# Kernel tuning notes

Hardware: AMD Instinct MI355X
Metric: run time of the kernel (lower is better)

Reference implementation:

```python
import jax, jax.numpy as jnp
import numpy as np

D_MODEL = 1024
NUM_HEADS = 16
HEAD_DIM = D_MODEL // NUM_HEADS
BATCH, SEQ = 2, 2048


def setup_inputs() -> dict:
    key = jax.random.key(0)
    ks = jax.random.split(key, 11)
    s = 1.0 / np.sqrt(D_MODEL)
    inp = {
        "query": jax.random.normal(ks[0], (BATCH, SEQ, D_MODEL), jnp.float32),
        "key": jax.random.normal(ks[1], (BATCH, SEQ, D_MODEL), jnp.float32),
        "value": jax.random.normal(ks[2], (BATCH, SEQ, D_MODEL), jnp.float32),
        "q_w": jax.random.uniform(ks[3], (D_MODEL, D_MODEL), jnp.float32, -s, s),
        "q_b": jax.random.uniform(ks[4], (D_MODEL,), jnp.float32, -s, s),
        "k_w": jax.random.uniform(ks[5], (D_MODEL, D_MODEL), jnp.float32, -s, s),
        "k_b": jax.random.uniform(ks[6], (D_MODEL,), jnp.float32, -s, s),
        "v_w": jax.random.uniform(ks[7], (D_MODEL, D_MODEL), jnp.float32, -s, s),
        "v_b": jax.random.uniform(ks[8], (D_MODEL,), jnp.float32, -s, s),
        "o_w": jax.random.uniform(ks[9], (D_MODEL, D_MODEL), jnp.float32, -s, s),
        "o_b": jax.random.uniform(ks[10], (D_MODEL,), jnp.float32, -s, s),
    }
    return inp


def reference(query, key, value, q_w, q_b, k_w, k_b, v_w, v_b, o_w, o_b):
    B = query.shape[0]
    # linear projections (torch Linear: x @ W^T + b)
    q = query @ q_w.T + q_b
    k = key @ k_w.T + k_b
    v = value @ v_w.T + v_b
    # split heads: [B, S, D] -> [B, H, S, Hd]
    def split(x):
        return x.reshape(B, -1, NUM_HEADS, HEAD_DIM).transpose(0, 2, 1, 3)
    q, k, v = split(q), split(k), split(v)
    scores = jnp.einsum("bhqd,bhkd->bhqk", q, k) / np.sqrt(HEAD_DIM).astype(np.float32)
    attn = jax.nn.softmax(scores, axis=-1)
    out = jnp.einsum("bhqk,bhkd->bhqd", attn, v)  # [B,H,S,Hd]
    merged = out.transpose(0, 2, 1, 3).reshape(B, -1, D_MODEL)
    return merged @ o_w.T + o_b
```

## Files before the change

### kernel.cpp

```cpp
#include <hip/hip_runtime.h>
#include <hip/hip_bf16.h>

typedef unsigned short u16;
typedef unsigned int u32;
typedef __attribute__((ext_vector_type(8))) short short8;
typedef __attribute__((ext_vector_type(4))) short s16x4;
typedef __attribute__((ext_vector_type(4))) float f32x4;
typedef __attribute__((ext_vector_type(4))) u32 u32v4;

__device__ __forceinline__ u16 f2bf(float f) {
    u32 u = __float_as_uint(f);
    return (u16)((u + 0x7FFFu + ((u >> 16) & 1u)) >> 16);
}
__device__ __forceinline__ u32 pack2bf(float a, float b) {
    __hip_bfloat162 h = __float22bfloat162_rn(float2{a, b});
    return *reinterpret_cast<u32*>(&h);
}
__device__ __forceinline__ float exp2hw(float x) {
    float r;
    asm("v_exp_f32 %0, %1" : "=v"(r) : "v"(x));
    return r;
}

__device__ __forceinline__ void gload16(const void* g, void* s) {
    __builtin_amdgcn_global_load_lds(
        (const __attribute__((address_space(1))) void*)g,
        (__attribute__((address_space(3))) void*)s, 16, 0, 0);
}

__global__ __launch_bounds__(256) void cast_w_kernel(
    const float* __restrict__ s0, const float* __restrict__ s1,
    const float* __restrict__ s2, const float* __restrict__ s3,
    u16* __restrict__ d0, u16* __restrict__ d1, u16* __restrict__ d2,
    u16* __restrict__ d3, int n)
{
    const int y = blockIdx.y;
    const float* s = y == 0 ? s0 : (y == 1 ? s1 : (y == 2 ? s2 : s3));
    u16* d = y == 0 ? d0 : (y == 1 ? d1 : (y == 2 ? d2 : d3));
    int i = (blockIdx.x * 256 + threadIdx.x) * 4;
    if (i < n) {
        float4 v = *(const float4*)(s + i);
        uint2 t;
        t.x = pack2bf(v.x, v.y);
        t.y = pack2bf(v.z, v.w);
        *(uint2*)(d + i) = t;
    }
}

__global__ __launch_bounds__(256) void qkv_gemm(
    const float* __restrict__ Xq, const float* __restrict__ Xk, const float* __restrict__ Xv,
    const u16* __restrict__ Wq, const u16* __restrict__ Wk, const u16* __restrict__ Wv,
    const float* __restrict__ qb, const float* __restrict__ kb, const float* __restrict__ vb,
    u16* __restrict__ Qo, u16* __restrict__ Ko, u16* __restrict__ Vo)
{
    constexpr int N = 1024, K = 1024;
    __shared__ __align__(16) u16 Asm[2][4096];
    __shared__ __align__(16) u16 Bsm[2][4096];
    const int z = blockIdx.z;
    const float* Afp = z == 0 ? Xq : (z == 1 ? Xk : Xv);
    const u16* W = z == 0 ? Wq : (z == 1 ? Wk : Wv);
    const float* bias = z == 0 ? qb : (z == 1 ? kb : vb);

    const int tid = threadIdx.x;
    const int wid = tid >> 6;
    const int lane = tid & 63;
    const int r15 = lane & 15, g = lane >> 4;
    const int fb = blockIdx.y * 8 + blockIdx.x;
    const int lsw = (fb & 7) * 32 + (fb >> 3);
    const int m0 = (lsw >> 3) * 128, n0 = (lsw & 7) * 128;
    const int wr = wid >> 1, wc = wid & 1;

    f32x4 acc[4][4];
#pragma unroll
    for (int i = 0; i < 4; ++i)
#pragma unroll
        for (int j = 0; j < 4; ++j) acc[i][j] = (f32x4){0.f, 0.f, 0.f, 0.f};

    const float* Abase = Afp + (size_t)(m0 + (tid >> 3)) * 1024 + (tid & 7) * 4;
    const int wboff = (tid >> 3) * 32 + (tid & 7) * 4;
    const int idx0 = tid, idx1 = tid + 256;
    const size_t boff0 = (size_t)(n0 + (idx0 >> 2)) * K + (idx0 & 3) * 8;
    const size_t boff1 = (size_t)(n0 + (idx1 >> 2)) * K + (idx1 & 3) * 8;
    const u16* abase = &Asm[0][0] + (wr * 64 + r15) * 32 + g * 8;
    const u16* bbase = &Bsm[0][0] + (wc * 64 + r15) * 32 + g * 8;

    float4 L[4];
#pragma unroll
    for (int c = 0; c < 4; ++c) L[c] = *(const float4*)(Abase + c * 32768);
    gload16(W + boff0, &Bsm[0][wid * 512]);
    gload16(W + boff1, &Bsm[0][2048 + wid * 512]);
    {
        u16* wb = &Asm[0][0] + wboff;
#pragma unroll
        for (int c = 0; c < 4; ++c) {
            uint2 t{pack2bf(L[c].x, L[c].y), pack2bf(L[c].z, L[c].w)};
            *(uint2*)(wb + c * 1024) = t;
        }
    }
    __syncthreads();

#pragma unroll 2
    for (int t = 0; t < 32; ++t) {
        const int buf = t & 1;
        if (t < 31) {
            const int kt = (t + 1) * 32;
#pragma unroll
            for (int c = 0; c < 4; ++c) L[c] = *(const float4*)(Abase + c * 32768 + kt);
            gload16(W + boff0 + kt, &Bsm[buf ^ 1][wid * 512]);
            gload16(W + boff1 + kt, &Bsm[buf ^ 1][2048 + wid * 512]);
        }
        short8 af[4], bfr[4];
#pragma unroll
        for (int i = 0; i < 4; ++i) {
            af[i]  = *(const short8*)(abase + buf * 4096 + i * 512);
            bfr[i] = *(const short8*)(bbase + buf * 4096 + i * 512);
        }
#pragma unroll
        for (int i = 0; i < 4; ++i)
#pragma unroll
            for (int j = 0; j < 4; ++j)
                acc[i][j] = __builtin_amdgcn_mfma_f32_16x16x32_bf16(af[i], bfr[j], acc[i][j], 0, 0, 0);
        if (t < 31) {
            u16* wb = &Asm[buf ^ 1][0] + wboff;
#pragma unroll
            for (int c = 0; c < 4; ++c) {
                uint2 tt{pack2bf(L[c].x, L[c].y), pack2bf(L[c].z, L[c].w)};
                *(uint2*)(wb + c * 1024) = tt;
            }
        }
        __syncthreads();
    }

    const float scale = (z == 0) ? 0.125f * 1.4426950408889634f : 1.0f;
    u16* ob = z == 0 ? Qo : (z == 1 ? Ko : Vo);
#pragma unroll
    for (int i = 0; i < 4; ++i) {
        const int mbase = m0 + wr * 64 + i * 16 + g * 4;
#pragma unroll
        for (int j = 0; j < 4; ++j) {
            const int n = n0 + wc * 64 + j * 16 + r15;
            const float bb = bias[n];
            if (z < 2) {
#pragma unroll
                for (int r = 0; r < 4; ++r)
                    ob[(size_t)(mbase + r) * N + n] = f2bf((acc[i][j][r] + bb) * scale);
            } else {
                const int b_ = mbase >> 11, s_ = mbase & 2047;
                const int blk = (s_ >> 2) & 7;
                const int pb = ((blk & 3) << 1) | (blk >> 2);
                const int s_new = (s_ & ~31) | (pb << 2);
                s16x4 pk;
#pragma unroll
                for (int r = 0; r < 4; ++r) pk[r] = (short)f2bf(acc[i][j][r] + bb);
                *(s16x4*)(ob + ((size_t)b_ << 21) + (size_t)n * 2048 + s_new) = pk;
            }
        }
    }
}

__global__ __launch_bounds__(256) void o_gemm(
    const u16* __restrict__ A, const u16* __restrict__ W,
    const float* __restrict__ bias, float* __restrict__ outp)
{
    constexpr int N = 1024, K = 1024;
    __shared__ __align__(16) u16 Asm[2][4096];
    __shared__ __align__(16) u16 Bsm[2][4096];
    const int tid = threadIdx.x;
    const int wid = tid >> 6;
    const int lane = tid & 63;
    const int r15 = lane & 15, g = lane >> 4;
    const int fb = blockIdx.y * 8 + blockIdx.x;
    const int lsw = (fb & 7) * 32 + (fb >> 3);
    const int m0 = (lsw >> 3) * 128, n0 = (lsw & 7) * 128;
    const int wr = wid >> 1, wc = wid & 1;

    f32x4 acc[4][4];
#pragma unroll
    for (int i = 0; i < 4; ++i)
#pragma unroll
        for (int j = 0; j < 4; ++j) acc[i][j] = (f32x4){0.f, 0.f, 0.f, 0.f};

    const int idx0 = tid, idx1 = tid + 256;
    const size_t aoff0 = (size_t)(m0 + (idx0 >> 2)) * K + (idx0 & 3) * 8;
    const size_t aoff1 = (size_t)(m0 + (idx1 >> 2)) * K + (idx1 & 3) * 8;
    const size_t boff0 = (size_t)(n0 + (idx0 >> 2)) * K + (idx0 & 3) * 8;
    const size_t boff1 = (size_t)(n0 + (idx1 >> 2)) * K + (idx1 & 3) * 8;
    const u16* abase = &Asm[0][0] + (wr * 64 + r15) * 32 + g * 8;
    const u16* bbase = &Bsm[0][0] + (wc * 64 + r15) * 32 + g * 8;

    gload16(A + aoff0, &Asm[0][wid * 512]);
    gload16(A + aoff1, &Asm[0][2048 + wid * 512]);
    gload16(W + boff0, &Bsm[0][wid * 512]);
    gload16(W + boff1, &Bsm[0][2048 + wid * 512]);
    __syncthreads();

#pragma unroll 2
    for (int t = 0; t < 32; ++t) {
        const int buf = t & 1;
        if (t < 31) {
            const int kt = (t + 1) * 32;
            gload16(A + aoff0 + kt, &Asm[buf ^ 1][wid * 512]);
            gload16(A + aoff1 + kt, &Asm[buf ^ 1][2048 + wid * 512]);
            gload16(W + boff0 + kt, &Bsm[buf ^ 1][wid * 512]);
            gload16(W + boff1 + kt, &Bsm[buf ^ 1][2048 + wid * 512]);
        }
        short8 af[4], bfr[4];
#pragma unroll
        for (int i = 0; i < 4; ++i) {
            af[i]  = *(const short8*)(abase + buf * 4096 + i * 512);
            bfr[i] = *(const short8*)(bbase + buf * 4096 + i * 512);
        }
#pragma unroll
        for (int i = 0; i < 4; ++i)
#pragma unroll
            for (int j = 0; j < 4; ++j)
                acc[i][j] = __builtin_amdgcn_mfma_f32_16x16x32_bf16(af[i], bfr[j], acc[i][j], 0, 0, 0);
        __syncthreads();
    }

#pragma unroll
    for (int i = 0; i < 4; ++i) {
        const int mbase = m0 + wr * 64 + i * 16 + g * 4;
#pragma unroll
        for (int j = 0; j < 4; ++j) {
            const int n = n0 + wc * 64 + j * 16 + r15;
            const float bb = bias[n];
#pragma unroll
            for (int r = 0; r < 4; ++r)
                outp[(size_t)(mbase + r) * N + n] = acc[i][j][r] + bb;
        }
    }
}

__global__ __launch_bounds__(256) void attn_kernel(
    const u16* __restrict__ Q, const u16* __restrict__ Kb,
    const u16* __restrict__ Vt, u16* __restrict__ Mo)
{
    __shared__ __align__(16) u16 Ksm[2][4096];
    __shared__ __align__(16) u16 Vsm[2][4096];
    const int tid = threadIdx.x;
    const int wid = tid >> 6, lane = tid & 63;
    const int r15 = lane & 15, g = lane >> 4;
    const int bid = blockIdx.x;
    const int l = (bid & 7) * 64 + (bid >> 3);
    const int bh = l >> 4;
    const int b = bh >> 4, h = bh & 15;
    const int q0 = (l & 15) * 128 + wid * 32;

    const u16* Qbase = Q + ((size_t)b * 2048 + q0) * 1024 + h * 64;
    short8 qf[2][2];
#pragma unroll
    for (int qt = 0; qt < 2; ++qt)
#pragma unroll
        for (int f = 0; f < 2; ++f)
            qf[qt][f] = *(const short8*)(Qbase + (size_t)(qt * 16 + r15) * 1024 + f * 32 + g * 8);

    const int p0 = tid, p1 = tid + 256;
    const int row0 = p0 >> 3, slot0s = (p0 & 7) ^ (row0 & 7);
    const int row1 = p1 >> 3, slot1s = (p1 & 7) ^ (row1 & 7);
    const u16* Ks0 = Kb + ((size_t)b * 2048 + row0) * 1024 + h * 64 + slot0s * 8;
    const u16* Ks1 = Kb + ((size_t)b * 2048 + row1) * 1024 + h * 64 + slot1s * 8;
    const u16* Vs0 = Vt + ((size_t)b << 21) + (size_t)(h * 64 + row0) * 2048 + slot0s * 8;
    const u16* Vs1 = Vt + ((size_t)b << 21) + (size_t)(h * 64 + row1) * 2048 + slot1s * 8;

    const int sA = r15 & 7;
    const int sl0 = (g ^ sA) * 8;
    const int sl1 = sl0 ^ 32;
    const u16* kb0 = &Ksm[0][0] + r15 * 64 + sl0;
    const u16* kb1 = &Ksm[0][0] + r15 * 64 + sl1;
    const u16* vb0 = &Vsm[0][0] + r15 * 64 + sl0;
    const u16* vb1 = &Vsm[0][0] + r15 * 64 + sl1;

    f32x4 acc[2][4];
#pragma unroll
    for (int qt = 0; qt < 2; ++qt)
#pragma unroll
        for (int d4 = 0; d4 < 4; ++d4) acc[qt][d4] = (f32x4){0.f, 0.f, 0.f, 0.f};
    f32x4 accl[2] = {(f32x4){0.f, 0.f, 0.f, 0.f}, (f32x4){0.f, 0.f, 0.f, 0.f}};
    const short8 vone = {0x3F80, 0x3F80, 0x3F80, 0x3F80, 0x3F80, 0x3F80, 0x3F80, 0x3F80};

    gload16(Ks0, &Ksm[0][wid * 512]);
    gload16(Ks1, &Ksm[0][2048 + wid * 512]);
    gload16(Vs0, &Vsm[0][wid * 512]);
    gload16(Vs1, &Vsm[0][2048 + wid * 512]);
    Ks0 += 65536; Ks1 += 65536; Vs0 += 64; Vs1 += 64;
    __syncthreads();

#pragma unroll 2
    for (int t = 0; t < 32; ++t) {
        const int buf = t & 1;
        if (t < 31) {
            gload16(Ks0, &Ksm[buf ^ 1][wid * 512]);
            gload16(Ks1, &Ksm[buf ^ 1][2048 + wid * 512]);
            gload16(Vs0, &Vsm[buf ^ 1][wid * 512]);
            gload16(Vs1, &Vsm[buf ^ 1][2048 + wid * 512]);
            Ks0 += 65536; Ks1 += 65536; Vs0 += 64; Vs1 += 64;
        }

        short8 kf[4][2];
#pragma unroll
        for (int kt = 0; kt < 4; ++kt) {
            kf[kt][0] = *(const short8*)(kb0 + buf * 4096 + kt * 1024);
            kf[kt][1] = *(const short8*)(kb1 + buf * 4096 + kt * 1024);
        }

        f32x4 st[2][4];
#pragma unroll
        for (int qt = 0; qt < 2; ++qt)
#pragma unroll
            for (int kt = 0; kt < 4; ++kt) {
                f32x4 zz = (f32x4){0.f, 0.f, 0.f, 0.f};
                zz = __builtin_amdgcn_mfma_f32_16x16x32_bf16(kf[kt][0], qf[qt][0], zz, 0, 0, 0);
                zz = __builtin_amdgcn_mfma_f32_16x16x32_bf16(kf[kt][1], qf[qt][1], zz, 0, 0, 0);
                st[qt][kt] = zz;
            }

        u32v4 pA[2], pB[2];
#pragma unroll
        for (int qt = 0; qt < 2; ++qt) {
#pragma unroll
            for (int kt = 0; kt < 4; ++kt) {
                float e0 = exp2hw(st[qt][kt][0]);
                float e1 = exp2hw(st[qt][kt][1]);
                float e2 = exp2hw(st[qt][kt][2]);
                float e3 = exp2hw(st[qt][kt][3]);
                u32 lo = pack2bf(e0, e1);
                u32 hi = pack2bf(e2, e3);
                if (kt < 2) { pA[qt][kt * 2] = lo; pA[qt][kt * 2 + 1] = hi; }
                else        { pB[qt][(kt - 2) * 2] = lo; pB[qt][(kt - 2) * 2 + 1] = hi; }
            }
        }

        accl[0] = __builtin_amdgcn_mfma_f32_16x16x32_bf16(vone, __builtin_bit_cast(short8, pA[0]), accl[0], 0, 0, 0);
        accl[0] = __builtin_amdgcn_mfma_f32_16x16x32_bf16(vone, __builtin_bit_cast(short8, pB[0]), accl[0], 0, 0, 0);
        accl[1] = __builtin_amdgcn_mfma_f32_16x16x32_bf16(vone, __builtin_bit_cast(short8, pA[1]), accl[1], 0, 0, 0);
        accl[1] = __builtin_amdgcn_mfma_f32_16x16x32_bf16(vone, __builtin_bit_cast(short8, pB[1]), accl[1], 0, 0, 0);

#pragma unroll
        for (int d4 = 0; d4 < 4; ++d4) {
            short8 vf0 = *(const short8*)(vb0 + buf * 4096 + d4 * 1024);
            short8 vf1 = *(const short8*)(vb1 + buf * 4096 + d4 * 1024);
            acc[0][d4] = __builtin_amdgcn_mfma_f32_16x16x32_bf16(vf0, __builtin_bit_cast(short8, pA[0]), acc[0][d4], 0, 0, 0);
            acc[0][d4] = __builtin_amdgcn_mfma_f32_16x16x32_bf16(vf1, __builtin_bit_cast(short8, pB[0]), acc[0][d4], 0, 0, 0);
            acc[1][d4] = __builtin_amdgcn_mfma_f32_16x16x32_bf16(vf0, __builtin_bit_cast(short8, pA[1]), acc[1][d4], 0, 0, 0);
            acc[1][d4] = __builtin_amdgcn_mfma_f32_16x16x32_bf16(vf1, __builtin_bit_cast(short8, pB[1]), acc[1][d4], 0, 0, 0);
        }
        __syncthreads();
    }

#pragma unroll
    for (int qt = 0; qt < 2; ++qt) {
        const float inv = 1.f / accl[qt][0];
        const size_t orow = ((size_t)b * 2048 + q0 + qt * 16 + r15) * 1024 + h * 64;
#pragma unroll
        for (int d4 = 0; d4 < 4; ++d4) {
            uint2 o;
            o.x = pack2bf(acc[qt][d4][0] * inv, acc[qt][d4][1] * inv);
            o.y = pack2bf(acc[qt][d4][2] * inv, acc[qt][d4][3] * inv);
            *(uint2*)(Mo + orow + d4 * 16 + g * 4) = o;
        }
    }
}

extern "C" void kernel_launch(void* const* d_in, const int* in_sizes, int n_in,
                              void* d_out, int out_size, void* d_ws, size_t ws_size,
                              hipStream_t stream) {
    (void)in_sizes; (void)n_in; (void)out_size; (void)ws_size;
    const float* query = (const float*)d_in[0];
    const float* key   = (const float*)d_in[1];
    const float* value = (const float*)d_in[2];
    const float* q_w = (const float*)d_in[3];
    const float* q_b = (const float*)d_in[4];
    const float* k_w = (const float*)d_in[5];
    const float* k_b = (const float*)d_in[6];
    const float* v_w = (const float*)d_in[7];
    const float* v_b = (const float*)d_in[8];
    const float* o_w = (const float*)d_in[9];
    const float* o_b = (const float*)d_in[10];

    const size_t NE = (size_t)4096 * 1024;
    const size_t MW = (size_t)1024 * 1024;
    u16* w = (u16*)d_ws;
    u16* Wq = w;
    u16* Wk = Wq + MW;
    u16* Wv = Wk + MW;
    u16* Wo = Wv + MW;
    u16* Qb = Wo + MW;
    u16* Kb = Qb + NE;
    u16* Vt = Kb + NE;
    u16* Mo = Vt + NE;

    cast_w_kernel<<<dim3(1024, 4), 256, 0, stream>>>(
        q_w, k_w, v_w, o_w, Wq, Wk, Wv, Wo, (int)MW);
    qkv_gemm<<<dim3(8, 32, 3), 256, 0, stream>>>(
        query, key, value, Wq, Wk, Wv, q_b, k_b, v_b, Qb, Kb, Vt);
    attn_kernel<<<dim3(512), 256, 0, stream>>>(Qb, Kb, Vt, Mo);
    o_gemm<<<dim3(8, 32), 256, 0, stream>>>(Mo, Wo, o_b, (float*)d_out);
}
```

Baseline: 139.8 us.

## Pre-cast QKV activations to bf16 and load both GEMM operands via direct-to-LDS

The float32 activations are now cast to bf16 in one combined cast kernel together with the weights. The QKV GEMM then loads both A and B tiles with global_load_lds instead of staging A through registers and converting in-loop. The GEMM launch is flattened to a 1D grid of 768 blocks with a new swizzle, treating the concatenated Q/K/V weights as one N=3072 matrix. This removes the in-loop conversion and the register round trip, but adds an extra full pass over the activations (fp32 read, bf16 write and read back) plus more workspace memory.

```diff
diff --git a/kernel.cpp b/kernel.cpp
--- a/kernel.cpp
+++ b/kernel.cpp
@@ -28,17 +28,21 @@
         (__attribute__((address_space(3))) void*)s, 16, 0, 0);
 }
 
-__global__ __launch_bounds__(256) void cast_w_kernel(
-    const float* __restrict__ s0, const float* __restrict__ s1,
-    const float* __restrict__ s2, const float* __restrict__ s3,
+__global__ __launch_bounds__(256) void cast_all_kernel(
+    const float* __restrict__ s0, const float* __restrict__ s1, const float* __restrict__ s2,
+    const float* __restrict__ s3, const float* __restrict__ s4, const float* __restrict__ s5,
+    const float* __restrict__ s6,
     u16* __restrict__ d0, u16* __restrict__ d1, u16* __restrict__ d2,
-    u16* __restrict__ d3, int n)
+    u16* __restrict__ d3, u16* __restrict__ d4, u16* __restrict__ d5,
+    u16* __restrict__ d6, int nBig, int nSmall)
 {
     const int y = blockIdx.y;
-    const float* s = y == 0 ? s0 : (y == 1 ? s1 : (y == 2 ? s2 : s3));
-    u16* d = y == 0 ? d0 : (y == 1 ? d1 : (y == 2 ? d2 : d3));
+    const float* s = y == 0 ? s0 : (y == 1 ? s1 : (y == 2 ? s2 : (y == 3 ? s3 : (y == 4 ? s4 : (y == 5 ? s5 : s6)))));
+    u16* d = y == 0 ? d0 : (y == 1 ? d1 : (y == 2 ? d2 : (y == 3 ? d3 : (y == 4 ? d4 : (y == 5 ? d5 : d6)))));
+    const int n = (y < 3) ? nBig : nSmall;
     int i = (blockIdx.x * 256 + threadIdx.x) * 4;
-    if (i < n) {
+    const int stride = gridDim.x * 256 * 4;
+    for (; i < n; i += stride) {
         float4 v = *(const float4*)(s + i);
         uint2 t;
         t.x = pack2bf(v.x, v.y);
@@ -48,26 +52,25 @@
 }
 
 __global__ __launch_bounds__(256) void qkv_gemm(
-    const float* __restrict__ Xq, const float* __restrict__ Xk, const float* __restrict__ Xv,
-    const u16* __restrict__ Wq, const u16* __restrict__ Wk, const u16* __restrict__ Wv,
+    const u16* __restrict__ Xq, const u16* __restrict__ Xk, const u16* __restrict__ Xv,
+    const u16* __restrict__ Wqkv,
     const float* __restrict__ qb, const float* __restrict__ kb, const float* __restrict__ vb,
     u16* __restrict__ Qo, u16* __restrict__ Ko, u16* __restrict__ Vo)
 {
-    constexpr int N = 1024, K = 1024;
+    constexpr int K = 1024;
     __shared__ __align__(16) u16 Asm[2][4096];
     __shared__ __align__(16) u16 Bsm[2][4096];
-    const int z = blockIdx.z;
-    const float* Afp = z == 0 ? Xq : (z == 1 ? Xk : Xv);
-    const u16* W = z == 0 ? Wq : (z == 1 ? Wk : Wv);
-    const float* bias = z == 0 ? qb : (z == 1 ? kb : vb);
 
     const int tid = threadIdx.x;
     const int wid = tid >> 6;
     const int lane = tid & 63;
     const int r15 = lane & 15, g = lane >> 4;
-    const int fb = blockIdx.y * 8 + blockIdx.x;
-    const int lsw = (fb & 7) * 32 + (fb >> 3);
-    const int m0 = (lsw >> 3) * 128, n0 = (lsw & 7) * 128;
+    const int flat = blockIdx.x;
+    const int wgid = (flat & 7) * 96 + (flat >> 3);
+    const int m0 = (wgid / 24) * 128;
+    const int nAll = (wgid % 24) * 128;
+    const int z = nAll >> 10;
+    const u16* A = z == 0 ? Xq : (z == 1 ? Xk : Xv);
     const int wr = wid >> 1, wc = wid & 1;
 
     f32x4 acc[4][4];
@@ -76,27 +79,18 @@
 #pragma unroll
         for (int j = 0; j < 4; ++j) acc[i][j] = (f32x4){0.f, 0.f, 0.f, 0.f};
 
-    const float* Abase = Afp + (size_t)(m0 + (tid >> 3)) * 1024 + (tid & 7) * 4;
-    const int wboff = (tid >> 3) * 32 + (tid & 7) * 4;
     const int idx0 = tid, idx1 = tid + 256;
-    const size_t boff0 = (size_t)(n0 + (idx0 >> 2)) * K + (idx0 & 3) * 8;
-    const size_t boff1 = (size_t)(n0 + (idx1 >> 2)) * K + (idx1 & 3) * 8;
+    const size_t aoff0 = (size_t)(m0 + (idx0 >> 2)) * K + (idx0 & 3) * 8;
+    const size_t aoff1 = (size_t)(m0 + (idx1 >> 2)) * K + (idx1 & 3) * 8;
+    const size_t boff0 = (size_t)(nAll + (idx0 >> 2)) * K + (idx0 & 3) * 8;
+    const size_t boff1 = (size_t)(nAll + (idx1 >> 2)) * K + (idx1 & 3) * 8;
     const u16* abase = &Asm[0][0] + (wr * 64 + r15) * 32 + g * 8;
     const u16* bbase = &Bsm[0][0] + (wc * 64 + r15) * 32 + g * 8;
 
-    float4 L[4];
-#pragma unroll
-    for (int c = 0; c < 4; ++c) L[c] = *(const float4*)(Abase + c * 32768);
-    gload16(W + boff0, &Bsm[0][wid * 512]);
-    gload16(W + boff1, &Bsm[0][2048 + wid * 512]);
-    {
-        u16* wb = &Asm[0][0] + wboff;
-#pragma unroll
-        for (int c = 0; c < 4; ++c) {
-            uint2 t{pack2bf(L[c].x, L[c].y), pack2bf(L[c].z, L[c].w)};
-            *(uint2*)(wb + c * 1024) = t;
-        }
-    }
+    gload16(A + aoff0, &Asm[0][wid * 512]);
+    gload16(A + aoff1, &Asm[0][2048 + wid * 512]);
+    gload16(Wqkv + boff0, &Bsm[0][wid * 512]);
+    gload16(Wqkv + boff1, &Bsm[0][2048 + wid * 512]);
     __syncthreads();
 
 #pragma unroll 2
@@ -104,10 +98,10 @@
         const int buf = t & 1;
         if (t < 31) {
             const int kt = (t + 1) * 32;
-#pragma unroll
-            for (int c = 0; c < 4; ++c) L[c] = *(const float4*)(Abase + c * 32768 + kt);
-            gload16(W + boff0 + kt, &Bsm[buf ^ 1][wid * 512]);
-            gload16(W + boff1 + kt, &Bsm[buf ^ 1][2048 + wid * 512]);
+            gload16(A + aoff0 + kt, &Asm[buf ^ 1][wid * 512]);
+            gload16(A + aoff1 + kt, &Asm[buf ^ 1][2048 + wid * 512]);
+            gload16(Wqkv + boff0 + kt, &Bsm[buf ^ 1][wid * 512]);
+            gload16(Wqkv + boff1 + kt, &Bsm[buf ^ 1][2048 + wid * 512]);
         }
         short8 af[4], bfr[4];
 #pragma unroll
@@ -120,30 +114,24 @@
 #pragma unroll
             for (int j = 0; j < 4; ++j)
                 acc[i][j] = __builtin_amdgcn_mfma_f32_16x16x32_bf16(af[i], bfr[j], acc[i][j], 0, 0, 0);
-        if (t < 31) {
-            u16* wb = &Asm[buf ^ 1][0] + wboff;
-#pragma unroll
-            for (int c = 0; c < 4; ++c) {
-                uint2 tt{pack2bf(L[c].x, L[c].y), pack2bf(L[c].z, L[c].w)};
-                *(uint2*)(wb + c * 1024) = tt;
-            }
-        }
         __syncthreads();
     }
 
     const float scale = (z == 0) ? 0.125f * 1.4426950408889634f : 1.0f;
     u16* ob = z == 0 ? Qo : (z == 1 ? Ko : Vo);
+    const float* bias = z == 0 ? qb : (z == 1 ? kb : vb);
+    const int nloc0 = nAll & 1023;
 #pragma unroll
     for (int i = 0; i < 4; ++i) {
         const int mbase = m0 + wr * 64 + i * 16 + g * 4;
 #pragma unroll
         for (int j = 0; j < 4; ++j) {
-            const int n = n0 + wc * 64 + j * 16 + r15;
+            const int n = nloc0 + wc * 64 + j * 16 + r15;
             const float bb = bias[n];
             if (z < 2) {
 #pragma unroll
                 for (int r = 0; r < 4; ++r)
-                    ob[(size_t)(mbase + r) * N + n] = f2bf((acc[i][j][r] + bb) * scale);
+                    ob[(size_t)(mbase + r) * 1024 + n] = f2bf((acc[i][j][r] + bb) * scale);
             } else {
                 const int b_ = mbase >> 11, s_ = mbase & 2047;
                 const int blk = (s_ >> 2) & 7;
@@ -381,7 +369,10 @@
     const size_t NE = (size_t)4096 * 1024;
     const size_t MW = (size_t)1024 * 1024;
     u16* w = (u16*)d_ws;
-    u16* Wq = w;
+    u16* Xq = w;
+    u16* Xk = Xq + NE;
+    u16* Xv = Xk + NE;
+    u16* Wq = Xv + NE;
     u16* Wk = Wq + MW;
     u16* Wv = Wk + MW;
     u16* Wo = Wv + MW;
@@ -390,10 +381,11 @@
     u16* Vt = Kb + NE;
     u16* Mo = Vt + NE;
 
-    cast_w_kernel<<<dim3(1024, 4), 256, 0, stream>>>(
-        q_w, k_w, v_w, o_w, Wq, Wk, Wv, Wo, (int)MW);
-    qkv_gemm<<<dim3(8, 32, 3), 256, 0, stream>>>(
-        query, key, value, Wq, Wk, Wv, q_b, k_b, v_b, Qb, Kb, Vt);
+    cast_all_kernel<<<dim3(2048, 7), 256, 0, stream>>>(
+        query, key, value, q_w, k_w, v_w, o_w,
+        Xq, Xk, Xv, Wq, Wk, Wv, Wo, (int)NE, (int)MW);
+    qkv_gemm<<<dim3(768), 256, 0, stream>>>(
+        Xq, Xk, Xv, Wq, q_b, k_b, v_b, Qb, Kb, Vt);
     attn_kernel<<<dim3(512), 256, 0, stream>>>(Qb, Kb, Vt, Mo);
     o_gemm<<<dim3(8, 32), 256, 0, stream>>>(Mo, Wo, o_b, (float*)d_out);
 }
```

After: 143.0 us. 1.02x slower.
